# Optimization experiments

Hardware: AMD Instinct MI355X
Metric: run time of the kernel (lower is better)

## Reference

```python
import jax, jax.numpy as jnp
import numpy as np

ACT_BIT = 8
W_BIT = 8
EPS = 1e-8


def ste_round(x):
    # straight-through round (matches torch STE quant autograd)
    return x + jax.lax.stop_gradient(jnp.round(x) - x)


def quant_act(x):
    """Per-tensor symmetric 8-bit activation quantization (HAWQ QuantAct)."""
    n = 2 ** (ACT_BIT - 1) - 1  # 127
    x_max = jax.lax.stop_gradient(jnp.max(jnp.abs(x)))
    scale = jnp.maximum(x_max, EPS) / n
    x_int = jnp.clip(ste_round(x / scale), -n - 1, n)
    return x_int * scale, scale


def quant_linear(x_q, act_scale, weight, bias):
    """Per-channel symmetric 8-bit weight quant + integer matmul + fused dequant."""
    n = 2 ** (W_BIT - 1) - 1  # 127
    w_max = jax.lax.stop_gradient(jnp.max(jnp.abs(weight), axis=1, keepdims=True))  # [out,1]
    w_scale = jnp.maximum(w_max, EPS) / n                                            # [out,1]
    w_int = jnp.clip(ste_round(weight / w_scale), -n - 1, n)                         # [out,in]
    bias_scale = w_scale[:, 0] * act_scale                                           # [out]
    b_int = ste_round(bias / bias_scale)                                             # [out]
    x_int = x_q / act_scale                                   # integer-valued float, [..., in]
    out_int = jnp.einsum('...i,oi->...o', x_int, w_int)       # int8-domain GEMM in float
    return (out_int + b_int) * bias_scale                     # fused dequant


def setup_inputs() -> dict:
    key = jax.random.key(0)
    k1, k2, k3 = jax.random.split(key, 3)
    L, B, Q, D, O = 6, 8, 1024, 1024, 1024
    hs = jax.random.normal(k1, (L, B, Q, D), dtype=jnp.float32)
    weight = jax.random.normal(k2, (O, D), dtype=jnp.float32) * 0.02
    bias = jax.random.normal(k3, (O,), dtype=jnp.float32) * 0.02
    return {"hs": hs, "weight": weight, "bias": bias}


def reference(hs, weight, bias):
    x_q, act_scale = quant_act(hs)
    return quant_linear(x_q, act_scale, weight, bias)
```

## Files before the change

### kernel.cpp

```cpp
#include <hip/hip_runtime.h>
#include <stdint.h>

typedef int i32x4 __attribute__((ext_vector_type(4)));

#define K_DIM 1024
#define BM 256
#define BN 256
#define NKT 16


__device__ __forceinline__ int quant1(float v, float inv) {
  float t = rintf(v * inv);
  t = fminf(fmaxf(t, -128.0f), 127.0f);
  return (int)t;
}

__device__ __forceinline__ void gld_lds16(const signed char* g, signed char* l) {
  typedef const __attribute__((address_space(1))) unsigned int* gp_t;
  typedef __attribute__((address_space(3))) unsigned int* lp_t;
  __builtin_amdgcn_global_load_lds((gp_t)(const void*)g, (lp_t)(void*)l, 16, 0, 0);
}

#define SB __builtin_amdgcn_sched_barrier(0)
#define BAR __builtin_amdgcn_s_barrier()
#define WAIT_LGKM0 asm volatile("s_waitcnt lgkmcnt(0)" ::: "memory")

__global__ void absmax_part(const float* __restrict__ x, float* __restrict__ parts,
                            long long n4) {
  long long i = (long long)blockIdx.x * blockDim.x + threadIdx.x;
  const long long stride = (long long)gridDim.x * blockDim.x;
  const float4* x4 = (const float4*)x;
  float m = 0.0f;
  for (; i < n4; i += stride) {
    float4 v = x4[i];
    m = fmaxf(m, fmaxf(fmaxf(fabsf(v.x), fabsf(v.y)), fmaxf(fabsf(v.z), fabsf(v.w))));
  }
#pragma unroll
  for (int off = 32; off > 0; off >>= 1) m = fmaxf(m, __shfl_down(m, off, 64));
  __shared__ float sm[4];
  const int lane = threadIdx.x & 63, wid = threadIdx.x >> 6;
  if (lane == 0) sm[wid] = m;
  __syncthreads();
  if (threadIdx.x == 0)
    parts[blockIdx.x] = fmaxf(fmaxf(sm[0], sm[1]), fmaxf(sm[2], sm[3]));
}

__global__ void absmax_fin(const float* __restrict__ parts, unsigned int* __restrict__ amax_u,
                           int nparts) {
  const int t = threadIdx.x;
  float m = 0.0f;
  for (int i = t; i < nparts; i += 256) m = fmaxf(m, parts[i]);
#pragma unroll
  for (int off = 32; off > 0; off >>= 1) m = fmaxf(m, __shfl_down(m, off, 64));
  __shared__ float sm[4];
  const int lane = t & 63, wid = t >> 6;
  if (lane == 0) sm[wid] = m;
  __syncthreads();
  if (t == 0)
    amax_u[0] = __float_as_uint(fmaxf(fmaxf(sm[0], sm[1]), fmaxf(sm[2], sm[3])));
}

__global__ void wquant_kernel(const float* __restrict__ w, const float* __restrict__ bias,
                              const unsigned int* __restrict__ amax_u,
                              signed char* __restrict__ wq,
                              float* __restrict__ bscale, float* __restrict__ bint) {
  const int o = blockIdx.x;
  const int t = threadIdx.x;
  float4 v = ((const float4*)(w + (size_t)o * K_DIM))[t];
  float m = fmaxf(fmaxf(fabsf(v.x), fabsf(v.y)), fmaxf(fabsf(v.z), fabsf(v.w)));
#pragma unroll
  for (int off = 32; off > 0; off >>= 1) m = fmaxf(m, __shfl_down(m, off, 64));
  __shared__ float sm[4];
  __shared__ float s_scale;
  const int lane = t & 63, wid = t >> 6;
  if (lane == 0) sm[wid] = m;
  __syncthreads();
  if (t == 0) {
    float wm = fmaxf(fmaxf(sm[0], sm[1]), fmaxf(sm[2], sm[3]));
    float wsc = fmaxf(wm, 1e-8f) / 127.0f;
    float asc = fmaxf(__uint_as_float(*amax_u), 1e-8f) / 127.0f;
    float bsc = wsc * asc;
    bscale[o] = bsc;
    bint[o] = rintf(bias[o] / bsc);
    s_scale = wsc;
  }
  __syncthreads();
  const float inv = 1.0f / s_scale;
  int q0 = quant1(v.x, inv), q1 = quant1(v.y, inv), q2 = quant1(v.z, inv), q3 = quant1(v.w, inv);
  unsigned int p = (unsigned)(q0 & 255) | ((unsigned)(q1 & 255) << 8) |
                   ((unsigned)(q2 & 255) << 16) | ((unsigned)(q3 & 255) << 24);
  const int F = o >> 4, T = t >> 4;
  const int l = (((t >> 2) & 3) << 4) | (o & 15);
  const int j = (t << 2) & 15;
  *(unsigned int*)(wq + (((size_t)F << 14) + (T << 10) + (l << 4) + j)) = p;
}

__global__ void aquant_kernel(const float* __restrict__ x, const unsigned int* __restrict__ amax_u,
                              uint4* __restrict__ q16, int nchunk) {
  const float asc = fmaxf(__uint_as_float(*amax_u), 1e-8f) / 127.0f;
  const float inv = 1.0f / asc;
  int c = blockIdx.x * blockDim.x + threadIdx.x;
  const int stride = gridDim.x * blockDim.x;
  for (; c < nchunk; c += stride) {
    const int l = c & 63, T = (c >> 6) & 15, F = c >> 10;
    const size_t src = (((size_t)(F << 4) + (l & 15)) << 10) + (T << 6) + ((l >> 4) << 4);
    const float4* s4 = (const float4*)(x + src);
    unsigned int r[4];
#pragma unroll
    for (int q = 0; q < 4; q++) {
      float4 v = s4[q];
      int q0 = quant1(v.x, inv), q1 = quant1(v.y, inv), q2 = quant1(v.z, inv), q3 = quant1(v.w, inv);
      r[q] = (unsigned)(q0 & 255) | ((unsigned)(q1 & 255) << 8) |
             ((unsigned)(q2 & 255) << 16) | ((unsigned)(q3 & 255) << 24);
    }
    q16[c] = make_uint4(r[0], r[1], r[2], r[3]);
  }
}

__global__ __launch_bounds__(512, 2) void gemm_kernel(
    const signed char* __restrict__ A, const signed char* __restrict__ W,
    const float* __restrict__ bscale, const float* __restrict__ bint,
    float* __restrict__ out, int M, int N, int K) {
  extern __shared__ __align__(16) signed char smem[];
  signed char* Abase = smem;

  const int nwg = gridDim.x;
  const int orig = blockIdx.x;
  const int wgid = (orig & 7) * (nwg >> 3) + (orig >> 3);
  const int nbn = N / BN;
  const int bm = wgid / nbn;
  const int bn = wgid % nbn;
  const int m0 = bm * BM, n0 = bn * BN;

  const int tid = threadIdx.x;
  const int lane = tid & 63;
  const int wid = tid >> 6;
  const int wr = wid >> 2;
  const int wc = wid & 3;

  const signed char* gaf = A + (((size_t)(m0 >> 4) + wid) << 14) + (lane << 4);
  const size_t fs8 = (size_t)8 << 14;
  const signed char* gbf = W + (((size_t)(n0 >> 4) + wc * 4) << 14) + (lane << 4);

  i32x4 acc[8][4];
#pragma unroll
  for (int i = 0; i < 8; i++)
#pragma unroll
    for (int j = 0; j < 4; j++) acc[i][j] = (i32x4){0, 0, 0, 0};

  i32x4 afA[8], afB[8];
  i32x4 bfA[4], bfB[4];

#define LOADB(L, tt)                                                           \
  do {                                                                         \
    L[0] = *(const i32x4*)(gbf + ((size_t)0 << 14) + ((tt) << 10));            \
    L[1] = *(const i32x4*)(gbf + ((size_t)1 << 14) + ((tt) << 10));            \
    L[2] = *(const i32x4*)(gbf + ((size_t)2 << 14) + ((tt) << 10));            \
    L[3] = *(const i32x4*)(gbf + ((size_t)3 << 14) + ((tt) << 10));            \
  } while (0)

#define ISSUEA(tt)                                                             \
  do {                                                                         \
    gld_lds16(gaf + ((size_t)(tt) << 10),                                      \
              Abase + ((((tt) & 3) * 16 + wid) << 10));                        \
    gld_lds16(gaf + fs8 + ((size_t)(tt) << 10),                                \
              Abase + ((((tt) & 3) * 16 + wid + 8) << 10));                    \
  } while (0)

#define RD_A8(t, AF)                                                           \
  do {                                                                         \
    _Pragma("unroll") for (int i_ = 0; i_ < 8; i_++)                           \
      AF[i_] = *(const i32x4*)(Abase + ((((t) & 3) * 16 + wr * 8 + i_) << 10)  \
                               + (lane << 4));                                 \
  } while (0)

#define MFMA32(AF, U)                                                          \
  do {                                                                         \
    __builtin_amdgcn_s_setprio(1);                                             \
    _Pragma("unroll") for (int i_ = 0; i_ < 8; i_++)                           \
      _Pragma("unroll") for (int j_ = 0; j_ < 4; j_++)                         \
        acc[i_][j_] = __builtin_amdgcn_mfma_i32_16x16x64_i8(                   \
            AF[i_], U[j_], acc[i_][j_], 0, 0, 0);                              \
    __builtin_amdgcn_s_setprio(0);                                             \
  } while (0)

#define BODY(t, CA, NA, CB, NB, DORD, DOA, DOB, VMW)                           \
  do {                                                                         \
    asm volatile("s_waitcnt " VMW ::: "memory");                               \
    SB; BAR; SB;                                                               \
    if (DORD) RD_A8((t) + 1, NA);                                              \
    if (DOA) ISSUEA((t) + 3);                                                  \
    if (DOB) LOADB(NB, (t) + 1);                                               \
    MFMA32(CA, CB);                                                            \
  } while (0)

  ISSUEA(0); ISSUEA(1); ISSUEA(2);
  LOADB(bfA, 0);
  asm volatile("s_waitcnt vmcnt(8)" ::: "memory");
  SB; BAR; SB;
  RD_A8(0, afA);

  BODY(0,  afA, afB, bfA, bfB, 1, 1, 1, "vmcnt(6)");
  BODY(1,  afB, afA, bfB, bfA, 1, 1, 1, "vmcnt(6)");
  BODY(2,  afA, afB, bfA, bfB, 1, 1, 1, "vmcnt(6)");
  BODY(3,  afB, afA, bfB, bfA, 1, 1, 1, "vmcnt(6)");
  BODY(4,  afA, afB, bfA, bfB, 1, 1, 1, "vmcnt(6)");
  BODY(5,  afB, afA, bfB, bfA, 1, 1, 1, "vmcnt(6)");
  BODY(6,  afA, afB, bfA, bfB, 1, 1, 1, "vmcnt(6)");
  BODY(7,  afB, afA, bfB, bfA, 1, 1, 1, "vmcnt(6)");
  BODY(8,  afA, afB, bfA, bfB, 1, 1, 1, "vmcnt(6)");
  BODY(9,  afB, afA, bfB, bfA, 1, 1, 1, "vmcnt(6)");
  BODY(10, afA, afB, bfA, bfB, 1, 1, 1, "vmcnt(6)");
  BODY(11, afB, afA, bfB, bfA, 1, 1, 1, "vmcnt(6)");
  BODY(12, afA, afB, bfA, bfB, 1, 1, 1, "vmcnt(6)");
  BODY(13, afB, afA, bfB, bfA, 1, 0, 1, "vmcnt(6)");
  BODY(14, afA, afB, bfA, bfB, 1, 0, 1, "vmcnt(4)");
  BODY(15, afB, afA, bfB, bfA, 0, 0, 0, "vmcnt(4)");

  SB; BAR; SB;

#undef BODY
#undef MFMA32
#undef RD_A8
#undef ISSUEA
#undef LOADB

  float* Cst = (float*)smem;
  const int rr = (lane >> 4) * 4;
  const int cc = lane & 15;
#pragma unroll
  for (int q = 0; q < 4; ++q) {
    if (wr == (q >> 1)) {
#pragma unroll
      for (int j = 0; j < 4; j++) {
        const int colL = wc * 64 + j * 16 + cc;
        const float bs = bscale[n0 + colL];
        const float bi = bint[n0 + colL];
#pragma unroll
        for (int i2 = 0; i2 < 4; i2++) {
          const int i = (q & 1) * 4 + i2;
#pragma unroll
          for (int r = 0; r < 4; r++)
            Cst[(i2 * 16 + rr + r) * 256 + colL] = ((float)acc[i][j][r] + bi) * bs;
        }
      }
    }
    WAIT_LGKM0;
    BAR;
    const size_t rowbase = (size_t)(m0 + q * 64) * N + n0;
#pragma unroll
    for (int it = 0; it < 8; ++it) {
      const int r_ = it * 8 + wid;
      float4 v = *(const float4*)&Cst[r_ * 256 + lane * 4];
      *(float4*)&out[rowbase + (size_t)r_ * N + lane * 4] = v;
    }
    WAIT_LGKM0;
    BAR;
  }
}

extern "C" void kernel_launch(void* const* d_in, const int* in_sizes, int n_in,
                              void* d_out, int out_size, void* d_ws, size_t ws_size,
                              hipStream_t stream) {
  const float* hs = (const float*)d_in[0];
  const float* w = (const float*)d_in[1];
  const float* bias = (const float*)d_in[2];
  float* out = (float*)d_out;

  const long long n = (long long)in_sizes[0];
  const int K = K_DIM;
  const int O = in_sizes[2];
  const int M = (int)(n / K);

  char* ws = (char*)d_ws;
  unsigned int* amax_u = (unsigned int*)ws;
  float* parts = (float*)(ws + 1024);
  float* bscale = (float*)(ws + 16384);
  float* bint = (float*)(ws + 20480);
  signed char* wq = (signed char*)(ws + 65536);
  signed char* xq = (signed char*)(ws + 65536 + 1048576);

  hipFuncSetAttribute((const void*)gemm_kernel,
                      hipFuncAttributeMaxDynamicSharedMemorySize, 65536);

  const long long n4 = n / 4;
  absmax_part<<<2048, 256, 0, stream>>>(hs, parts, n4);
  absmax_fin<<<1, 256, 0, stream>>>(parts, amax_u, 2048);
  wquant_kernel<<<O, 256, 0, stream>>>(w, bias, amax_u, wq, bscale, bint);
  const int nchunk = (int)(n / 16);
  aquant_kernel<<<2048, 256, 0, stream>>>(hs, amax_u, (uint4*)xq, nchunk);

  const int nblocks = (M / BM) * (O / BN);
  gemm_kernel<<<nblocks, 512, 65536, stream>>>(xq, wq, bscale, bint, out, M, O, K);
}
```

Baseline: 179.5 us.

## Deepen A-tile LDS ring to six stages and barrier once per two k-steps

The A-tile LDS ring buffer grows from 4 to 6 stages (shared memory from 64KB to 96KB), and prefetch distance rises from 3 to 4 k-tiles. The main loop now issues a workgroup barrier every two k-steps instead of every step. A-fragment double buffering in registers is removed: each step reads its own A fragments from LDS just before the MFMAs. The aim is fewer barriers and more latency hiding, at the cost of more LDS (which may lower occupancy) and exposed LDS read latency before the MFMAs.

```diff
diff --git a/kernel.cpp b/kernel.cpp
--- a/kernel.cpp
+++ b/kernel.cpp
@@ -148,7 +148,7 @@
 #pragma unroll
     for (int j = 0; j < 4; j++) acc[i][j] = (i32x4){0, 0, 0, 0};
 
-  i32x4 afA[8], afB[8];
+  i32x4 af[8];
   i32x4 bfA[4], bfB[4];
 
 #define LOADB(L, tt)                                                           \
@@ -162,60 +162,66 @@
 #define ISSUEA(tt)                                                             \
   do {                                                                         \
     gld_lds16(gaf + ((size_t)(tt) << 10),                                      \
-              Abase + ((((tt) & 3) * 16 + wid) << 10));                        \
+              Abase + ((((tt) % 6) * 16 + wid) << 10));                        \
     gld_lds16(gaf + fs8 + ((size_t)(tt) << 10),                                \
-              Abase + ((((tt) & 3) * 16 + wid + 8) << 10));                    \
-  } while (0)
-
-#define RD_A8(t, AF)                                                           \
+              Abase + ((((tt) % 6) * 16 + wid + 8) << 10));                    \
+  } while (0)
+
+#define RD_A8(t)                                                               \
   do {                                                                         \
     _Pragma("unroll") for (int i_ = 0; i_ < 8; i_++)                           \
-      AF[i_] = *(const i32x4*)(Abase + ((((t) & 3) * 16 + wr * 8 + i_) << 10)  \
+      af[i_] = *(const i32x4*)(Abase + ((((t) % 6) * 16 + wr * 8 + i_) << 10)  \
                                + (lane << 4));                                 \
   } while (0)
 
-#define MFMA32(AF, U)                                                          \
+#define MFMA32(U)                                                              \
   do {                                                                         \
     __builtin_amdgcn_s_setprio(1);                                             \
     _Pragma("unroll") for (int i_ = 0; i_ < 8; i_++)                           \
       _Pragma("unroll") for (int j_ = 0; j_ < 4; j_++)                         \
         acc[i_][j_] = __builtin_amdgcn_mfma_i32_16x16x64_i8(                   \
-            AF[i_], U[j_], acc[i_][j_], 0, 0, 0);                              \
+            af[i_], U[j_], acc[i_][j_], 0, 0, 0);                              \
     __builtin_amdgcn_s_setprio(0);                                             \
   } while (0)
 
-#define BODY(t, CA, NA, CB, NB, DORD, DOA, DOB, VMW)                           \
-  do {                                                                         \
-    asm volatile("s_waitcnt " VMW ::: "memory");                               \
-    SB; BAR; SB;                                                               \
-    if (DORD) RD_A8((t) + 1, NA);                                              \
-    if (DOA) ISSUEA((t) + 3);                                                  \
-    if (DOB) LOADB(NB, (t) + 1);                                               \
-    MFMA32(CA, CB);                                                            \
-  } while (0)
-
-  ISSUEA(0); ISSUEA(1); ISSUEA(2);
+#define BODY(t, U, L, DOB, DOA, VMW, DOVM)                                     \
+  do {                                                                         \
+    if (DOB) LOADB(L, (t) + 1);                                                \
+    if (DOA) ISSUEA((t) + 4);                                                  \
+    SB;                                                                        \
+    RD_A8(t);                                                                  \
+    MFMA32(U);                                                                 \
+    if (DOVM) { asm volatile("s_waitcnt " VMW ::: "memory"); }                 \
+  } while (0)
+
   LOADB(bfA, 0);
-  asm volatile("s_waitcnt vmcnt(8)" ::: "memory");
-  SB; BAR; SB;
-  RD_A8(0, afA);
-
-  BODY(0,  afA, afB, bfA, bfB, 1, 1, 1, "vmcnt(6)");
-  BODY(1,  afB, afA, bfB, bfA, 1, 1, 1, "vmcnt(6)");
-  BODY(2,  afA, afB, bfA, bfB, 1, 1, 1, "vmcnt(6)");
-  BODY(3,  afB, afA, bfB, bfA, 1, 1, 1, "vmcnt(6)");
-  BODY(4,  afA, afB, bfA, bfB, 1, 1, 1, "vmcnt(6)");
-  BODY(5,  afB, afA, bfB, bfA, 1, 1, 1, "vmcnt(6)");
-  BODY(6,  afA, afB, bfA, bfB, 1, 1, 1, "vmcnt(6)");
-  BODY(7,  afB, afA, bfB, bfA, 1, 1, 1, "vmcnt(6)");
-  BODY(8,  afA, afB, bfA, bfB, 1, 1, 1, "vmcnt(6)");
-  BODY(9,  afB, afA, bfB, bfA, 1, 1, 1, "vmcnt(6)");
-  BODY(10, afA, afB, bfA, bfB, 1, 1, 1, "vmcnt(6)");
-  BODY(11, afB, afA, bfB, bfA, 1, 1, 1, "vmcnt(6)");
-  BODY(12, afA, afB, bfA, bfB, 1, 1, 1, "vmcnt(6)");
-  BODY(13, afB, afA, bfB, bfA, 1, 0, 1, "vmcnt(6)");
-  BODY(14, afA, afB, bfA, bfB, 1, 0, 1, "vmcnt(4)");
-  BODY(15, afB, afA, bfB, bfA, 0, 0, 0, "vmcnt(4)");
+  ISSUEA(0); ISSUEA(1); ISSUEA(2); ISSUEA(3);
+  asm volatile("s_waitcnt vmcnt(6)" ::: "memory");
+  SB; BAR; SB;
+
+  BODY(0,  bfA, bfB, 1, 1, "vmcnt(8)", 1);
+  BODY(1,  bfB, bfA, 1, 1, "vmcnt(8)", 1);
+  SB; BAR; SB;
+  BODY(2,  bfA, bfB, 1, 1, "vmcnt(8)", 1);
+  BODY(3,  bfB, bfA, 1, 1, "vmcnt(8)", 1);
+  SB; BAR; SB;
+  BODY(4,  bfA, bfB, 1, 1, "vmcnt(8)", 1);
+  BODY(5,  bfB, bfA, 1, 1, "vmcnt(8)", 1);
+  SB; BAR; SB;
+  BODY(6,  bfA, bfB, 1, 1, "vmcnt(8)", 1);
+  BODY(7,  bfB, bfA, 1, 1, "vmcnt(8)", 1);
+  SB; BAR; SB;
+  BODY(8,  bfA, bfB, 1, 1, "vmcnt(8)", 1);
+  BODY(9,  bfB, bfA, 1, 1, "vmcnt(8)", 1);
+  SB; BAR; SB;
+  BODY(10, bfA, bfB, 1, 1, "vmcnt(8)", 1);
+  BODY(11, bfB, bfA, 1, 1, "vmcnt(8)", 1);
+  SB; BAR; SB;
+  BODY(12, bfA, bfB, 1, 0, "vmcnt(6)", 1);
+  BODY(13, bfB, bfA, 1, 0, "vmcnt(4)", 1);
+  SB; BAR; SB;
+  BODY(14, bfA, bfB, 1, 0, "vmcnt(4)", 1);
+  BODY(15, bfB, bfA, 0, 0, "vmcnt(0)", 1);
 
   SB; BAR; SB;
 
@@ -281,7 +287,7 @@
   signed char* xq = (signed char*)(ws + 65536 + 1048576);
 
   hipFuncSetAttribute((const void*)gemm_kernel,
-                      hipFuncAttributeMaxDynamicSharedMemorySize, 65536);
+                      hipFuncAttributeMaxDynamicSharedMemorySize, 98304);
 
   const long long n4 = n / 4;
   absmax_part<<<2048, 256, 0, stream>>>(hs, parts, n4);
@@ -291,5 +297,5 @@
   aquant_kernel<<<2048, 256, 0, stream>>>(hs, amax_u, (uint4*)xq, nchunk);
 
   const int nblocks = (M / BM) * (O / BN);
-  gemm_kernel<<<nblocks, 512, 65536, stream>>>(xq, wq, bscale, bint, out, M, O, K);
-}
+  gemm_kernel<<<nblocks, 512, 98304, stream>>>(xq, wq, bscale, bint, out, M, O, K);
+}
```

Result: no change. 176.5 us, median of 2 (-1.6%).
